# Kernel optimization log

Measured on AMD Instinct MI355X. Metric: run time of the kernel, lower is better.

The kernel has to match this reference:

```python
import jax, jax.numpy as jnp
import numpy as np
from jax import lax

EPS = 1e-6  # LayerNorm2d eps


def _ln2d(x, w, b):
    # channel-wise LayerNorm over dim 1 of [B,C,H,W]
    mu = jnp.mean(x, axis=1, keepdims=True)
    var = jnp.mean((x - mu) ** 2, axis=1, keepdims=True)
    return (x - mu) / jnp.sqrt(var + EPS) * w[None, :, None, None] + b[None, :, None, None]


def _conv1x1(x, w, b):
    # w: [O, C]
    return jnp.einsum('bchw,oc->bohw', x, w) + b[None, :, None, None]


def _dconv(x, w, b):
    # 3x3 conv, dilation 4, padding 4 -> same H,W. w: [O, C, 3, 3]
    y = lax.conv_general_dilated(x, w, window_strides=(1, 1),
                                 padding=((4, 4), (4, 4)), rhs_dilation=(4, 4),
                                 dimension_numbers=('NCHW', 'OIHW', 'NCHW'))
    return y + b[None, :, None, None]


def _forward(x_l, x_r, nl_w, nl_b, nr_w, nr_b, lp1_w, lp1_b, rp1_w, rp1_b,
             dl_w, dl_b, dr_w, dr_b, lp2_w, lp2_b, rp2_w, rp2_b, beta, gamma):
    c = x_l.shape[1]
    scale = c ** (-0.5)
    N_l = _ln2d(x_l, nl_w, nl_b)
    N_r = _ln2d(x_r, nr_w, nr_b)
    V_l = jnp.transpose(_conv1x1(x_l, lp2_w, lp2_b), (0, 2, 3, 1))   # [B,H,W,C]
    V_r = jnp.transpose(_conv1x1(x_r, rp2_w, rp2_b), (0, 2, 3, 1))
    Q_l = jnp.transpose(_conv1x1(N_l, lp1_w, lp1_b), (0, 2, 3, 1))   # [B,H,W,C]
    Q_r = jnp.transpose(_conv1x1(N_r, rp1_w, rp1_b), (0, 2, 3, 1))
    K_l_T = jnp.transpose(_dconv(N_l, dl_w, dl_b), (0, 2, 1, 3))     # [B,H,C,W]
    K_r_T = jnp.transpose(_dconv(N_r, dr_w, dr_b), (0, 2, 1, 3))
    # per-row cross attention: [B,H,W,W]
    attn_r2l = jnp.einsum('bhwc,bhcv->bhwv', Q_l, K_r_T) * scale
    attn_l2r = jnp.einsum('bhwc,bhcv->bhwv', Q_r, K_l_T) * scale
    F_r2l = jnp.einsum('bhwv,bhvc->bhwc', jax.nn.softmax(attn_r2l, axis=-1), V_r)
    F_l2r = jnp.einsum('bhwv,bhvc->bhwc', jax.nn.softmax(attn_l2r, axis=-1), V_l)
    F_r2l = jnp.transpose(F_r2l, (0, 3, 1, 2)) * beta   # [B,C,H,W]
    F_l2r = jnp.transpose(F_l2r, (0, 3, 1, 2)) * gamma
    return x_l + F_r2l, x_r + F_l2r


def setup_inputs() -> dict:
    key = jax.random.key(0)
    ks = jax.random.split(key, 12)
    B, C, H, W = 2, 128, 192, 512
    s = 0.02
    rn = lambda k, shp: s * jax.random.normal(k, shp, jnp.float32)
    return {
        'x_l': jax.random.normal(ks[0], (B, C, H, W), jnp.float32),
        'x_r': jax.random.normal(ks[1], (B, C, H, W), jnp.float32),
        'nl_w': jnp.ones((C,), jnp.float32), 'nl_b': jnp.zeros((C,), jnp.float32),
        'nr_w': jnp.ones((C,), jnp.float32), 'nr_b': jnp.zeros((C,), jnp.float32),
        'lp1_w': rn(ks[2], (C, C)), 'lp1_b': jnp.zeros((C,), jnp.float32),
        'rp1_w': rn(ks[3], (C, C)), 'rp1_b': jnp.zeros((C,), jnp.float32),
        'dl_w': rn(ks[4], (C, C, 3, 3)), 'dl_b': jnp.zeros((C,), jnp.float32),
        'dr_w': rn(ks[5], (C, C, 3, 3)), 'dr_b': jnp.zeros((C,), jnp.float32),
        'lp2_w': rn(ks[6], (C, C)), 'lp2_b': jnp.zeros((C,), jnp.float32),
        'rp2_w': rn(ks[7], (C, C)), 'rp2_b': jnp.zeros((C,), jnp.float32),
        'beta': 0.1 * jax.random.normal(ks[8], (1, C, 1, 1), jnp.float32),
        'gamma': 0.1 * jax.random.normal(ks[9], (1, C, 1, 1), jnp.float32),
    }


def reference(x_l, x_r, nl_w, nl_b, nr_w, nr_b, lp1_w, lp1_b, rp1_w, rp1_b,
              dl_w, dl_b, dr_w, dr_b, lp2_w, lp2_b, rp2_w, rp2_b, beta, gamma):
    return _forward(x_l, x_r, nl_w, nl_b, nr_w, nr_b, lp1_w, lp1_b, rp1_w, rp1_b,
                    dl_w, dl_b, dr_w, dr_b, lp2_w, lp2_b, rp2_w, rp2_b, beta, gamma)
```

## Files before the change

### kernel.cpp

```cpp
#include <hip/hip_runtime.h>
#include <stdint.h>

#define CC 128
#define HH 192
#define WW 512
#define BB 2
#define HW (HH*WW)
#define CHW (CC*HW)
#define TENS (BB*CHW)

typedef __attribute__((ext_vector_type(8))) short bf16x8;
typedef __attribute__((ext_vector_type(4))) float f32x4;
typedef __attribute__((ext_vector_type(4))) unsigned short u16x4;

__device__ __forceinline__ unsigned short f2bf(float f) {
    union { float f; unsigned u; } v; v.f = f;
    return (unsigned short)((v.u + 0x7FFFu + ((v.u >> 16) & 1u)) >> 16);
}
__device__ __forceinline__ float bf2f(unsigned short u) {
    union { unsigned u; float f; } v; v.u = ((unsigned)u) << 16;
    return v.f;
}
__device__ __forceinline__ uint32_t cvtpk(float lo, float hi) {
    uint32_t r;
    asm("v_cvt_pk_bf16_f32 %0, %1, %2" : "=v"(r) : "v"(lo), "v"(hi));
    return r;
}
__device__ __forceinline__ f32x4 MFMA(bf16x8 a, bf16x8 b, f32x4 c) {
    return __builtin_amdgcn_mfma_f32_16x16x32_bf16(a, b, c, 0, 0, 0);
}

__global__ __launch_bounds__(256) void wcast_k(
    const float* __restrict__ dlw, const float* __restrict__ drw,
    unsigned short* __restrict__ wd)
{
    int i = blockIdx.x * 256 + threadIdx.x;
    if (i >= 2 * 9 * CC * CC) return;
    int side = i / (9 * CC * CC);
    int r = i % (9 * CC * CC);
    int tap = r / (CC * CC);
    int r2 = r % (CC * CC);
    int o = r2 >> 7, c = r2 & 127;
    const float* src = side ? drw : dlw;
    wd[i] = f2bf(src[((size_t)o * CC + c) * 9 + tap]);
}

__global__ __launch_bounds__(256) void lnv_k(
    const float* __restrict__ xl, const float* __restrict__ xr,
    const float* __restrict__ nlw, const float* __restrict__ nlb,
    const float* __restrict__ nrw, const float* __restrict__ nrb,
    const float* __restrict__ wlp, const float* __restrict__ blp,
    const float* __restrict__ wrp, const float* __restrict__ brp,
    unsigned short* __restrict__ ntl, unsigned short* __restrict__ ntr,
    unsigned short* __restrict__ vlo, unsigned short* __restrict__ vro)
{
    const int side = blockIdx.y;
    const float* x  = side ? xr : xl;
    const float* nw = side ? nrw : nlw;
    const float* nb = side ? nrb : nlb;
    const float* wv = side ? wrp : wlp;
    const float* bv = side ? brp : blp;
    unsigned short* nt = side ? ntr : ntl;
    unsigned short* vo = side ? vro : vlo;
    const int bid = blockIdx.x;
    const int wt = bid & 7, h = (bid >> 3) % HH, b = bid / (8 * HH);
    const int w0 = wt * 64;
    const int t = threadIdx.x;

    __shared__ unsigned short sA[64][136];
    __shared__ unsigned short sB[128][136];
    __shared__ float red[8][64];
    __shared__ float smu[64], srs[64];

    {
        const int w = t & 63, cg = t >> 6;
        const float* xp = x + (size_t)b * CHW + (size_t)h * WW + w0 + w;
        float s = 0.f, q = 0.f;
        for (int i = 0; i < 16; i++) {
            int c = cg * 32 + i * 2;
            float v0 = xp[(size_t)c * HW];
            float v1 = xp[(size_t)(c + 1) * HW];
            ushort2 u; u.x = f2bf(v0); u.y = f2bf(v1);
            *(ushort2*)&sA[w][c] = u;
            s += v0 + v1; q += v0 * v0 + v1 * v1;
        }
        red[cg][w] = s; red[4 + cg][w] = q;
    }
    for (int it = 0; it < 16; it++) {
        int f = it * 1024 + t * 4;
        int o = f >> 7, c = f & 127;
        float4 v = *(const float4*)(wv + o * CC + c);
        sB[o][c] = f2bf(v.x); sB[o][c + 1] = f2bf(v.y);
        sB[o][c + 2] = f2bf(v.z); sB[o][c + 3] = f2bf(v.w);
    }
    __syncthreads();
    if (t < 64) {
        float S = red[0][t] + red[1][t] + red[2][t] + red[3][t];
        float Q = red[4][t] + red[5][t] + red[6][t] + red[7][t];
        float mu = S * (1.f / CC);
        float var = fmaxf(Q * (1.f / CC) - mu * mu, 0.f);
        smu[t] = mu; srs[t] = rsqrtf(var + 1e-6f);
    }
    __syncthreads();
    {
        const int w = t >> 2, c0 = (t & 3) * 32;
        const float mu = smu[w], rs = srs[w];
        unsigned short* np = nt + ((size_t)(b * HH + h) * WW + w0 + w) * CC;
        for (int i = 0; i < 32; i += 2) {
            int c = c0 + i;
            float v0 = (bf2f(sA[w][c]) - mu) * rs * nw[c] + nb[c];
            float v1 = (bf2f(sA[w][c + 1]) - mu) * rs * nw[c + 1] + nb[c + 1];
            ushort2 u; u.x = f2bf(v0); u.y = f2bf(v1);
            *(ushort2*)&np[c] = u;
        }
    }
    const int wid = t >> 6, l = t & 63, lr = l & 15, lg = l >> 4;
    f32x4 acc[8] = {};
    for (int kk = 0; kk < 4; kk++) {
        bf16x8 a = *(const bf16x8*)&sA[wid * 16 + lr][kk * 32 + lg * 8];
#pragma unroll
        for (int n_ = 0; n_ < 8; n_++) {
            bf16x8 bb = *(const bf16x8*)&sB[n_ * 16 + lr][kk * 32 + lg * 8];
            acc[n_] = MFMA(a, bb, acc[n_]);
        }
    }
    unsigned short* vp = vo + ((size_t)(b * HH + h) * CC) * WW + w0;
    for (int n_ = 0; n_ < 8; n_++) {
        int o = n_ * 16 + lr;
        float bias = bv[o];
        u16x4 u;
        u[0] = f2bf(acc[n_][0] + bias);
        u[1] = f2bf(acc[n_][1] + bias);
        u[2] = f2bf(acc[n_][2] + bias);
        u[3] = f2bf(acc[n_][3] + bias);
        *(u16x4*)&vp[(size_t)o * WW + wid * 16 + lg * 4] = u;
    }
}

__global__ __launch_bounds__(256) void dconv_k(
    const unsigned short* __restrict__ ntl, const unsigned short* __restrict__ ntr,
    const unsigned short* __restrict__ wd,
    const float* __restrict__ dlb, const float* __restrict__ drb,
    unsigned short* __restrict__ klo, unsigned short* __restrict__ kro)
{
    const int side = blockIdx.y;
    const unsigned short* nt = side ? ntr : ntl;
    const unsigned short* wdp = wd + (size_t)side * 9 * CC * CC;
    const float* bd = side ? drb : dlb;
    unsigned short* ko = side ? kro : klo;
    const int bid0 = blockIdx.x;
    const int lgc = (bid0 & 7) * 192 + (bid0 >> 3);
    const int wt = lgc & 3;
    const int hb = lgc >> 2;
    const int h = hb % HH, b = hb / HH;
    const int w0 = wt * 128;
    const int t = threadIdx.x;
    const int wid = t >> 6, l = t & 63, lr = l & 15, lg = l >> 4;

    __shared__ unsigned short sA[136][136];
    __shared__ unsigned short sB[128][136];

    f32x4 acc[2][8] = {};
    for (int dy = 0; dy < 3; dy++) {
        const int hh = h + 4 * (dy - 1);
        const bool hok = (hh >= 0 && hh < HH);
        __syncthreads();
        for (int f = t * 8; f < 136 * 128; f += 2048) {
            int wloc = f >> 7, c = f & 127;
            int w = w0 - 4 + wloc;
            bf16x8 v = {0, 0, 0, 0, 0, 0, 0, 0};
            if (hok && w >= 0 && w < WW)
                v = *(const bf16x8*)(nt + ((size_t)(b * HH + hh) * WW + w) * CC + c);
            *(bf16x8*)&sA[wloc][c] = v;
        }
        for (int dx = 0; dx < 3; dx++) {
            __syncthreads();
            const int tap = dy * 3 + dx;
            for (int it = 0; it < 8; it++) {
                int f = it * 2048 + t * 8;
                *(bf16x8*)&sB[f >> 7][f & 127] =
                    *(const bf16x8*)(wdp + (size_t)tap * CC * CC + f);
            }
            __syncthreads();
            const int ar = wid * 16 + lr + 4 * dx;
            for (int kk = 0; kk < 4; kk++) {
                bf16x8 a0 = *(const bf16x8*)&sA[ar][kk * 32 + lg * 8];
                bf16x8 a1 = *(const bf16x8*)&sA[64 + ar][kk * 32 + lg * 8];
#pragma unroll
                for (int n_ = 0; n_ < 8; n_++) {
                    bf16x8 bb = *(const bf16x8*)&sB[n_ * 16 + lr][kk * 32 + lg * 8];
                    acc[0][n_] = MFMA(a0, bb, acc[0][n_]);
                    acc[1][n_] = MFMA(a1, bb, acc[1][n_]);
                }
            }
        }
    }
    unsigned short* kp = ko + ((size_t)(b * HH + h) * WW + w0) * CC;
    for (int mi = 0; mi < 2; mi++)
        for (int n_ = 0; n_ < 8; n_++) {
            int o = n_ * 16 + lr;
            float bias = bd[o];
            for (int j = 0; j < 4; j++) {
                int w = mi * 64 + wid * 16 + lg * 4 + j;
                kp[(size_t)w * CC + o] = f2bf(acc[mi][n_][j] + bias);
            }
        }
}

__global__ __launch_bounds__(256, 3) void attn_k(
    const unsigned short* __restrict__ ntl, const unsigned short* __restrict__ ntr,
    const unsigned short* __restrict__ kl,  const unsigned short* __restrict__ kr,
    const unsigned short* __restrict__ vtl, const unsigned short* __restrict__ vtr,
    const float* __restrict__ lp1w, const float* __restrict__ lp1b,
    const float* __restrict__ rp1w, const float* __restrict__ rp1b,
    const float* __restrict__ xl, const float* __restrict__ xr,
    const float* __restrict__ beta, const float* __restrict__ gamma,
    float* __restrict__ out)
{
    __shared__ __align__(16) char smem[53248];
    unsigned short* sQ  = (unsigned short*)smem;
    unsigned short* sW  = (unsigned short*)(smem + 17408);
    unsigned short* sKt = (unsigned short*)(smem + 17408);
    unsigned short* sVt = (unsigned short*)(smem + 34816);

    const int dir = blockIdx.z;
    const unsigned short* nq  = dir ? ntr : ntl;
    const unsigned short* kws = dir ? kl : kr;
    const unsigned short* vws = dir ? vtl : vtr;
    const float* wq   = dir ? rp1w : lp1w;
    const float* bq   = dir ? rp1b : lp1b;
    const float* xres = dir ? xr : xl;
    const float* mult = dir ? gamma : beta;
    float* op = out + (size_t)dir * TENS;

    const int bid = blockIdx.x;
    const int xcd = bid & 7;
    const int s   = bid >> 3;
    const int qb  = s & 7;
    const int bh  = xcd + 8 * (s >> 3);
    const int q0  = qb * 64;
    const int t = threadIdx.x;
    const int wid = t >> 6, l = t & 63, lr = l & 15, lg = l >> 4;

    const unsigned short* ksrc = kws + (size_t)bh * WW * CC;
    const unsigned short* vsrc = vws + (size_t)bh * CC * WW;

    bf16x8 kreg[4], vreg[4];
#pragma unroll
    for (int it = 0; it < 4; it++) {
        int f = it * 2048 + t * 8;
        kreg[it] = *(const bf16x8*)(ksrc + f);
    }
#pragma unroll
    for (int it = 0; it < 4; it++) {
        int f = it * 2048 + t * 8;
        int c = f >> 6, k = f & 63;
        vreg[it] = *(const bf16x8*)(vsrc + (size_t)c * WW + k);
    }

    {
        const unsigned short* nsrc = nq + ((size_t)bh * WW + q0) * CC;
        for (int it = 0; it < 4; it++) {
            int f = it * 2048 + t * 8;
            *(bf16x8*)&sQ[(f >> 7) * 136 + (f & 127)] = *(const bf16x8*)(nsrc + f);
        }
        for (int it = 0; it < 16; it++) {
            int f = it * 1024 + t * 4;
            int o = f >> 7, c = f & 127;
            float4 v = *(const float4*)(wq + o * CC + c);
            unsigned short* p = &sW[o * 136 + c];
            p[0] = f2bf(v.x); p[1] = f2bf(v.y); p[2] = f2bf(v.z); p[3] = f2bf(v.w);
        }
    }
    __syncthreads();
    f32x4 qacc[8] = {};
    for (int kk = 0; kk < 4; kk++) {
        bf16x8 a = *(const bf16x8*)&sQ[(wid * 16 + lr) * 136 + kk * 32 + lg * 8];
#pragma unroll
        for (int n_ = 0; n_ < 8; n_++) {
            bf16x8 b = *(const bf16x8*)&sW[(n_ * 16 + lr) * 136 + kk * 32 + lg * 8];
            qacc[n_] = MFMA(a, b, qacc[n_]);
        }
    }
    const float SCL = 0.08838834764831845f * 1.4426950408889634f;
    for (int n_ = 0; n_ < 8; n_++) {
        float bias = bq[n_ * 16 + lr];
        for (int j = 0; j < 4; j++)
            sQ[(wid * 16 + lg * 4 + j) * 136 + n_ * 16 + lr] =
                f2bf((qacc[n_][j] + bias) * SCL);
    }
    __syncthreads();
    bf16x8 qf[4];
#pragma unroll
    for (int kk = 0; kk < 4; kk++)
        qf[kk] = *(const bf16x8*)&sQ[(wid * 16 + lr) * 136 + kk * 32 + lg * 8];

    f32x4 oacc[8] = {};
    float mrow = -1e30f, lrow = 0.f;
    const int src0 = lr + ((l & 16) << 1);
    const int src1 = src0 + 16;
    const int hi = lg >> 1;

    for (int kb = 0; kb < 8; kb++) {
        __syncthreads();
#pragma unroll
        for (int it = 0; it < 4; it++) {
            int f = it * 2048 + t * 8;
            *(bf16x8*)&sKt[(f >> 7) * 136 + (f & 127)] = kreg[it];
        }
#pragma unroll
        for (int it = 0; it < 4; it++) {
            int f = it * 2048 + t * 8;
            int c = f >> 6, k = f & 63;
            *(bf16x8*)&sVt[c * 72 + k] = vreg[it];
        }
        if (kb < 7) {
#pragma unroll
            for (int it = 0; it < 4; it++) {
                int f = it * 2048 + t * 8;
                kreg[it] = *(const bf16x8*)(ksrc + (kb + 1) * 64 * CC + f);
            }
#pragma unroll
            for (int it = 0; it < 4; it++) {
                int f = it * 2048 + t * 8;
                int c = f >> 6, k = f & 63;
                vreg[it] = *(const bf16x8*)(vsrc + (size_t)c * WW + (kb + 1) * 64 + k);
            }
        }
        __syncthreads();
        f32x4 sacc[4] = {};
        __builtin_amdgcn_s_setprio(1);
        for (int kk = 0; kk < 4; kk++)
#pragma unroll
            for (int n_ = 0; n_ < 4; n_++) {
                bf16x8 kf = *(const bf16x8*)&sKt[(n_ * 16 + lr) * 136 + kk * 32 + lg * 8];
                sacc[n_] = MFMA(kf, qf[kk], sacc[n_]);
            }
        __builtin_amdgcn_s_setprio(0);
        float pm = sacc[0][0];
#pragma unroll
        for (int n_ = 0; n_ < 4; n_++)
#pragma unroll
            for (int j = 0; j < 4; j++) pm = fmaxf(pm, sacc[n_][j]);
        pm = fmaxf(pm, __shfl_xor(pm, 16, 64));
        pm = fmaxf(pm, __shfl_xor(pm, 32, 64));
        float mn = fmaxf(mrow, pm);
        float al = exp2f(mrow - mn);
        mrow = mn;
        float p[4][4];
        float rs = 0.f;
#pragma unroll
        for (int n_ = 0; n_ < 4; n_++)
#pragma unroll
            for (int j = 0; j < 4; j++) {
                p[n_][j] = exp2f(sacc[n_][j] - mn);
                rs += p[n_][j];
            }
        rs += __shfl_xor(rs, 16, 64);
        rs += __shfl_xor(rs, 32, 64);
        lrow = lrow * al + rs;
#pragma unroll
        for (int n_ = 0; n_ < 8; n_++) {
            f32x4 o = oacc[n_];
            o[0] *= al; o[1] *= al; o[2] *= al; o[3] *= al;
            oacc[n_] = o;
        }
        uint32_t pa0 = cvtpk(p[0][0], p[0][1]), pa1 = cvtpk(p[0][2], p[0][3]);
        uint32_t pb0 = cvtpk(p[1][0], p[1][1]), pb1 = cvtpk(p[1][2], p[1][3]);
        uint32_t pc0 = cvtpk(p[2][0], p[2][1]), pc1 = cvtpk(p[2][2], p[2][3]);
        uint32_t pd0 = cvtpk(p[3][0], p[3][1]), pd1 = cvtpk(p[3][2], p[3][3]);
        {
            uint32_t q00 = __shfl(pa0, src0, 64);
            uint32_t q01 = __shfl(pa1, src0, 64);
            uint32_t q02 = __shfl(pa0, src1, 64);
            uint32_t q03 = __shfl(pa1, src1, 64);
            uint32_t q10 = __shfl(pb0, src0, 64);
            uint32_t q11 = __shfl(pb1, src0, 64);
            uint32_t q12 = __shfl(pb0, src1, 64);
            uint32_t q13 = __shfl(pb1, src1, 64);
            union { uint32_t u[4]; bf16x8 v; } pf;
            pf.u[0] = hi ? q10 : q00;
            pf.u[1] = hi ? q11 : q01;
            pf.u[2] = hi ? q12 : q02;
            pf.u[3] = hi ? q13 : q03;
            __builtin_amdgcn_s_setprio(1);
#pragma unroll
            for (int n_ = 0; n_ < 8; n_++) {
                bf16x8 va = *(const bf16x8*)&sVt[(n_ * 16 + lr) * 72 + lg * 8];
                oacc[n_] = MFMA(va, pf.v, oacc[n_]);
            }
            __builtin_amdgcn_s_setprio(0);
        }
        {
            uint32_t q00 = __shfl(pc0, src0, 64);
            uint32_t q01 = __shfl(pc1, src0, 64);
            uint32_t q02 = __shfl(pc0, src1, 64);
            uint32_t q03 = __shfl(pc1, src1, 64);
            uint32_t q10 = __shfl(pd0, src0, 64);
            uint32_t q11 = __shfl(pd1, src0, 64);
            uint32_t q12 = __shfl(pd0, src1, 64);
            uint32_t q13 = __shfl(pd1, src1, 64);
            union { uint32_t u[4]; bf16x8 v; } pf;
            pf.u[0] = hi ? q10 : q00;
            pf.u[1] = hi ? q11 : q01;
            pf.u[2] = hi ? q12 : q02;
            pf.u[3] = hi ? q13 : q03;
            __builtin_amdgcn_s_setprio(1);
#pragma unroll
            for (int n_ = 0; n_ < 8; n_++) {
                bf16x8 va = *(const bf16x8*)&sVt[(n_ * 16 + lr) * 72 + 32 + lg * 8];
                oacc[n_] = MFMA(va, pf.v, oacc[n_]);
            }
            __builtin_amdgcn_s_setprio(0);
        }
    }

    const float inv = 1.f / lrow;
    const int b = bh / HH, h = bh % HH;
    const int w = q0 + wid * 16 + lr;
    const float* xp = xres + (size_t)b * CHW + (size_t)h * WW + w;
    float* outp = op + (size_t)b * CHW + (size_t)h * WW + w;
#pragma unroll
    for (int n_ = 0; n_ < 8; n_++)
#pragma unroll
        for (int j = 0; j < 4; j++) {
            int c = n_ * 16 + lg * 4 + j;
            outp[(size_t)c * HW] = xp[(size_t)c * HW] + oacc[n_][j] * inv * mult[c];
        }
}

extern "C" void kernel_launch(void* const* d_in, const int* in_sizes, int n_in,
                              void* d_out, int out_size, void* d_ws, size_t ws_size,
                              hipStream_t stream)
{
    const float* xl   = (const float*)d_in[0];
    const float* xr   = (const float*)d_in[1];
    const float* nlw  = (const float*)d_in[2];
    const float* nlb  = (const float*)d_in[3];
    const float* nrw  = (const float*)d_in[4];
    const float* nrb  = (const float*)d_in[5];
    const float* lp1w = (const float*)d_in[6];
    const float* lp1b = (const float*)d_in[7];
    const float* rp1w = (const float*)d_in[8];
    const float* rp1b = (const float*)d_in[9];
    const float* dlw  = (const float*)d_in[10];
    const float* dlb  = (const float*)d_in[11];
    const float* drw  = (const float*)d_in[12];
    const float* drb  = (const float*)d_in[13];
    const float* lp2w = (const float*)d_in[14];
    const float* lp2b = (const float*)d_in[15];
    const float* rp2w = (const float*)d_in[16];
    const float* rp2b = (const float*)d_in[17];
    const float* beta = (const float*)d_in[18];
    const float* gamma= (const float*)d_in[19];
    float* out = (float*)d_out;

    unsigned short* ws = (unsigned short*)d_ws;
    const size_t A = (size_t)TENS;
    unsigned short* Ntl = ws;
    unsigned short* Ntr = ws + A;
    unsigned short* Kl  = ws + 2 * A;
    unsigned short* Kr  = ws + 3 * A;
    unsigned short* Vtl = ws + 4 * A;
    unsigned short* Vtr = ws + 5 * A;
    unsigned short* Wd  = ws + 6 * A;

    wcast_k<<<dim3(1152), 256, 0, stream>>>(dlw, drw, Wd);
    lnv_k<<<dim3(3072, 2), 256, 0, stream>>>(xl, xr, nlw, nlb, nrw, nrb,
        lp2w, lp2b, rp2w, rp2b, Ntl, Ntr, Vtl, Vtr);
    dconv_k<<<dim3(1536, 2), 256, 0, stream>>>(Ntl, Ntr, Wd, dlb, drb, Kl, Kr);
    attn_k<<<dim3(3072, 1, 2), 256, 0, stream>>>(Ntl, Ntr, Kl, Kr, Vtl, Vtr,
        lp1w, lp1b, rp1w, rp1b, xl, xr, beta, gamma, out);
}
```

Before: 578.5 us.

## Double attention query tile per block and retile dconv warps as 2x2 output grid

The attention kernel now handles 128 queries per block (32 per warp, two MFMA query groups), so each staged K/V tile is reused across twice as many queries and the grid is halved. Shared memory grows and launch bounds drop to 2 blocks per CU. The dconv kernel splits warps into a 2x2 grid over width and output channels, loading 4 A and 4 B fragments for 16 MFMAs instead of 2 A and 8 B. Scalar bf16 conversions are replaced with packed cvtpk stores in several places.

```diff
diff --git a/kernel.cpp b/kernel.cpp
--- a/kernel.cpp
+++ b/kernel.cpp
@@ -80,8 +80,7 @@
             int c = cg * 32 + i * 2;
             float v0 = xp[(size_t)c * HW];
             float v1 = xp[(size_t)(c + 1) * HW];
-            ushort2 u; u.x = f2bf(v0); u.y = f2bf(v1);
-            *(ushort2*)&sA[w][c] = u;
+            *(uint32_t*)&sA[w][c] = cvtpk(v0, v1);
             s += v0 + v1; q += v0 * v0 + v1 * v1;
         }
         red[cg][w] = s; red[4 + cg][w] = q;
@@ -90,8 +89,8 @@
         int f = it * 1024 + t * 4;
         int o = f >> 7, c = f & 127;
         float4 v = *(const float4*)(wv + o * CC + c);
-        sB[o][c] = f2bf(v.x); sB[o][c + 1] = f2bf(v.y);
-        sB[o][c + 2] = f2bf(v.z); sB[o][c + 3] = f2bf(v.w);
+        *(uint32_t*)&sB[o][c]     = cvtpk(v.x, v.y);
+        *(uint32_t*)&sB[o][c + 2] = cvtpk(v.z, v.w);
     }
     __syncthreads();
     if (t < 64) {
@@ -110,8 +109,7 @@
             int c = c0 + i;
             float v0 = (bf2f(sA[w][c]) - mu) * rs * nw[c] + nb[c];
             float v1 = (bf2f(sA[w][c + 1]) - mu) * rs * nw[c + 1] + nb[c + 1];
-            ushort2 u; u.x = f2bf(v0); u.y = f2bf(v1);
-            *(ushort2*)&np[c] = u;
+            *(uint32_t*)&np[c] = cvtpk(v0, v1);
         }
     }
     const int wid = t >> 6, l = t & 63, lr = l & 15, lg = l >> 4;
@@ -128,12 +126,10 @@
     for (int n_ = 0; n_ < 8; n_++) {
         int o = n_ * 16 + lr;
         float bias = bv[o];
-        u16x4 u;
-        u[0] = f2bf(acc[n_][0] + bias);
-        u[1] = f2bf(acc[n_][1] + bias);
-        u[2] = f2bf(acc[n_][2] + bias);
-        u[3] = f2bf(acc[n_][3] + bias);
-        *(u16x4*)&vp[(size_t)o * WW + wid * 16 + lg * 4] = u;
+        uint2 uu;
+        uu.x = cvtpk(acc[n_][0] + bias, acc[n_][1] + bias);
+        uu.y = cvtpk(acc[n_][2] + bias, acc[n_][3] + bias);
+        *(uint2*)&vp[(size_t)o * WW + wid * 16 + lg * 4] = uu;
     }
 }
 
@@ -156,11 +152,12 @@
     const int w0 = wt * 128;
     const int t = threadIdx.x;
     const int wid = t >> 6, l = t & 63, lr = l & 15, lg = l >> 4;
+    const int whalf = wid & 1, ohalf = wid >> 1;
 
     __shared__ unsigned short sA[136][136];
     __shared__ unsigned short sB[128][136];
 
-    f32x4 acc[2][8] = {};
+    f32x4 acc[4][4] = {};
     for (int dy = 0; dy < 3; dy++) {
         const int hh = h + 4 * (dy - 1);
         const bool hok = (hh >= 0 && hh < HH);
@@ -182,32 +179,35 @@
                     *(const bf16x8*)(wdp + (size_t)tap * CC * CC + f);
             }
             __syncthreads();
-            const int ar = wid * 16 + lr + 4 * dx;
             for (int kk = 0; kk < 4; kk++) {
-                bf16x8 a0 = *(const bf16x8*)&sA[ar][kk * 32 + lg * 8];
-                bf16x8 a1 = *(const bf16x8*)&sA[64 + ar][kk * 32 + lg * 8];
-#pragma unroll
-                for (int n_ = 0; n_ < 8; n_++) {
-                    bf16x8 bb = *(const bf16x8*)&sB[n_ * 16 + lr][kk * 32 + lg * 8];
-                    acc[0][n_] = MFMA(a0, bb, acc[0][n_]);
-                    acc[1][n_] = MFMA(a1, bb, acc[1][n_]);
-                }
+                bf16x8 af[4], bf_[4];
+#pragma unroll
+                for (int g = 0; g < 4; g++)
+                    af[g] = *(const bf16x8*)&sA[whalf * 64 + g * 16 + lr + 4 * dx][kk * 32 + lg * 8];
+#pragma unroll
+                for (int n_ = 0; n_ < 4; n_++)
+                    bf_[n_] = *(const bf16x8*)&sB[ohalf * 64 + n_ * 16 + lr][kk * 32 + lg * 8];
+#pragma unroll
+                for (int g = 0; g < 4; g++)
+#pragma unroll
+                    for (int n_ = 0; n_ < 4; n_++)
+                        acc[g][n_] = MFMA(af[g], bf_[n_], acc[g][n_]);
             }
         }
     }
     unsigned short* kp = ko + ((size_t)(b * HH + h) * WW + w0) * CC;
-    for (int mi = 0; mi < 2; mi++)
-        for (int n_ = 0; n_ < 8; n_++) {
-            int o = n_ * 16 + lr;
+    for (int g = 0; g < 4; g++)
+        for (int n_ = 0; n_ < 4; n_++) {
+            int o = ohalf * 64 + n_ * 16 + lr;
             float bias = bd[o];
             for (int j = 0; j < 4; j++) {
-                int w = mi * 64 + wid * 16 + lg * 4 + j;
-                kp[(size_t)w * CC + o] = f2bf(acc[mi][n_][j] + bias);
-            }
-        }
-}
-
-__global__ __launch_bounds__(256, 3) void attn_k(
+                int w = whalf * 64 + g * 16 + lg * 4 + j;
+                kp[(size_t)w * CC + o] = f2bf(acc[g][n_][j] + bias);
+            }
+        }
+}
+
+__global__ __launch_bounds__(256, 2) void attn_k(
     const unsigned short* __restrict__ ntl, const unsigned short* __restrict__ ntr,
     const unsigned short* __restrict__ kl,  const unsigned short* __restrict__ kr,
     const unsigned short* __restrict__ vtl, const unsigned short* __restrict__ vtr,
@@ -217,11 +217,11 @@
     const float* __restrict__ beta, const float* __restrict__ gamma,
     float* __restrict__ out)
 {
-    __shared__ __align__(16) char smem[53248];
+    __shared__ __align__(16) char smem[70656];
     unsigned short* sQ  = (unsigned short*)smem;
-    unsigned short* sW  = (unsigned short*)(smem + 17408);
-    unsigned short* sKt = (unsigned short*)(smem + 17408);
-    unsigned short* sVt = (unsigned short*)(smem + 34816);
+    unsigned short* sW  = (unsigned short*)(smem + 34816);
+    unsigned short* sKt = (unsigned short*)(smem + 34816);
+    unsigned short* sVt = (unsigned short*)(smem + 52224);
 
     const int dir = blockIdx.z;
     const unsigned short* nq  = dir ? ntr : ntl;
@@ -236,9 +236,9 @@
     const int bid = blockIdx.x;
     const int xcd = bid & 7;
     const int s   = bid >> 3;
-    const int qb  = s & 7;
-    const int bh  = xcd + 8 * (s >> 3);
-    const int q0  = qb * 64;
+    const int qb  = s & 3;
+    const int bh  = xcd + 8 * (s >> 2);
+    const int q0  = qb * 128;
     const int t = threadIdx.x;
     const int wid = t >> 6, l = t & 63, lr = l & 15, lg = l >> 4;
 
@@ -260,7 +260,7 @@
 
     {
         const unsigned short* nsrc = nq + ((size_t)bh * WW + q0) * CC;
-        for (int it = 0; it < 4; it++) {
+        for (int it = 0; it < 8; it++) {
             int f = it * 2048 + t * 8;
             *(bf16x8*)&sQ[(f >> 7) * 136 + (f & 127)] = *(const bf16x8*)(nsrc + f);
         }
@@ -268,35 +268,47 @@
             int f = it * 1024 + t * 4;
             int o = f >> 7, c = f & 127;
             float4 v = *(const float4*)(wq + o * CC + c);
-            unsigned short* p = &sW[o * 136 + c];
-            p[0] = f2bf(v.x); p[1] = f2bf(v.y); p[2] = f2bf(v.z); p[3] = f2bf(v.w);
+            *(uint32_t*)&sW[o * 136 + c]     = cvtpk(v.x, v.y);
+            *(uint32_t*)&sW[o * 136 + c + 2] = cvtpk(v.z, v.w);
         }
     }
     __syncthreads();
-    f32x4 qacc[8] = {};
-    for (int kk = 0; kk < 4; kk++) {
-        bf16x8 a = *(const bf16x8*)&sQ[(wid * 16 + lr) * 136 + kk * 32 + lg * 8];
-#pragma unroll
-        for (int n_ = 0; n_ < 8; n_++) {
-            bf16x8 b = *(const bf16x8*)&sW[(n_ * 16 + lr) * 136 + kk * 32 + lg * 8];
-            qacc[n_] = MFMA(a, b, qacc[n_]);
-        }
-    }
-    const float SCL = 0.08838834764831845f * 1.4426950408889634f;
-    for (int n_ = 0; n_ < 8; n_++) {
-        float bias = bq[n_ * 16 + lr];
-        for (int j = 0; j < 4; j++)
-            sQ[(wid * 16 + lg * 4 + j) * 136 + n_ * 16 + lr] =
-                f2bf((qacc[n_][j] + bias) * SCL);
+    {
+        f32x4 qacc[2][8] = {};
+        for (int kk = 0; kk < 4; kk++) {
+            bf16x8 a0 = *(const bf16x8*)&sQ[(wid * 32 + lr) * 136 + kk * 32 + lg * 8];
+            bf16x8 a1 = *(const bf16x8*)&sQ[(wid * 32 + 16 + lr) * 136 + kk * 32 + lg * 8];
+#pragma unroll
+            for (int n_ = 0; n_ < 8; n_++) {
+                bf16x8 b = *(const bf16x8*)&sW[(n_ * 16 + lr) * 136 + kk * 32 + lg * 8];
+                qacc[0][n_] = MFMA(a0, b, qacc[0][n_]);
+                qacc[1][n_] = MFMA(a1, b, qacc[1][n_]);
+            }
+        }
+        const float SCL = 0.08838834764831845f * 1.4426950408889634f;
+        __syncthreads();
+#pragma unroll
+        for (int mg = 0; mg < 2; mg++)
+#pragma unroll
+            for (int n_ = 0; n_ < 8; n_++) {
+                float bias = bq[n_ * 16 + lr];
+#pragma unroll
+                for (int j = 0; j < 4; j++)
+                    sQ[(wid * 32 + mg * 16 + lg * 4 + j) * 136 + n_ * 16 + lr] =
+                        f2bf((qacc[mg][n_][j] + bias) * SCL);
+            }
     }
     __syncthreads();
-    bf16x8 qf[4];
-#pragma unroll
-    for (int kk = 0; kk < 4; kk++)
-        qf[kk] = *(const bf16x8*)&sQ[(wid * 16 + lr) * 136 + kk * 32 + lg * 8];
-
-    f32x4 oacc[8] = {};
-    float mrow = -1e30f, lrow = 0.f;
+    bf16x8 qf[2][4];
+#pragma unroll
+    for (int qg = 0; qg < 2; qg++)
+#pragma unroll
+        for (int kk = 0; kk < 4; kk++)
+            qf[qg][kk] = *(const bf16x8*)&sQ[(wid * 32 + qg * 16 + lr) * 136 + kk * 32 + lg * 8];
+
+    f32x4 oacc[8][2] = {};
+    float mrow[2] = {-1e30f, -1e30f};
+    float lrow[2] = {0.f, 0.f};
     const int src0 = lr + ((l & 16) << 1);
     const int src1 = src0 + 16;
     const int hi = lg >> 1;
@@ -328,105 +340,103 @@
             }
         }
         __syncthreads();
-        f32x4 sacc[4] = {};
+        f32x4 sacc[2][4] = {};
         __builtin_amdgcn_s_setprio(1);
         for (int kk = 0; kk < 4; kk++)
 #pragma unroll
             for (int n_ = 0; n_ < 4; n_++) {
                 bf16x8 kf = *(const bf16x8*)&sKt[(n_ * 16 + lr) * 136 + kk * 32 + lg * 8];
-                sacc[n_] = MFMA(kf, qf[kk], sacc[n_]);
+                sacc[0][n_] = MFMA(kf, qf[0][kk], sacc[0][n_]);
+                sacc[1][n_] = MFMA(kf, qf[1][kk], sacc[1][n_]);
             }
         __builtin_amdgcn_s_setprio(0);
-        float pm = sacc[0][0];
-#pragma unroll
-        for (int n_ = 0; n_ < 4; n_++)
-#pragma unroll
-            for (int j = 0; j < 4; j++) pm = fmaxf(pm, sacc[n_][j]);
-        pm = fmaxf(pm, __shfl_xor(pm, 16, 64));
-        pm = fmaxf(pm, __shfl_xor(pm, 32, 64));
-        float mn = fmaxf(mrow, pm);
-        float al = exp2f(mrow - mn);
-        mrow = mn;
-        float p[4][4];
-        float rs = 0.f;
-#pragma unroll
-        for (int n_ = 0; n_ < 4; n_++)
-#pragma unroll
-            for (int j = 0; j < 4; j++) {
-                p[n_][j] = exp2f(sacc[n_][j] - mn);
-                rs += p[n_][j];
-            }
-        rs += __shfl_xor(rs, 16, 64);
-        rs += __shfl_xor(rs, 32, 64);
-        lrow = lrow * al + rs;
-#pragma unroll
-        for (int n_ = 0; n_ < 8; n_++) {
-            f32x4 o = oacc[n_];
-            o[0] *= al; o[1] *= al; o[2] *= al; o[3] *= al;
-            oacc[n_] = o;
-        }
-        uint32_t pa0 = cvtpk(p[0][0], p[0][1]), pa1 = cvtpk(p[0][2], p[0][3]);
-        uint32_t pb0 = cvtpk(p[1][0], p[1][1]), pb1 = cvtpk(p[1][2], p[1][3]);
-        uint32_t pc0 = cvtpk(p[2][0], p[2][1]), pc1 = cvtpk(p[2][2], p[2][3]);
-        uint32_t pd0 = cvtpk(p[3][0], p[3][1]), pd1 = cvtpk(p[3][2], p[3][3]);
-        {
-            uint32_t q00 = __shfl(pa0, src0, 64);
-            uint32_t q01 = __shfl(pa1, src0, 64);
-            uint32_t q02 = __shfl(pa0, src1, 64);
-            uint32_t q03 = __shfl(pa1, src1, 64);
-            uint32_t q10 = __shfl(pb0, src0, 64);
-            uint32_t q11 = __shfl(pb1, src0, 64);
-            uint32_t q12 = __shfl(pb0, src1, 64);
-            uint32_t q13 = __shfl(pb1, src1, 64);
-            union { uint32_t u[4]; bf16x8 v; } pf;
-            pf.u[0] = hi ? q10 : q00;
-            pf.u[1] = hi ? q11 : q01;
-            pf.u[2] = hi ? q12 : q02;
-            pf.u[3] = hi ? q13 : q03;
+        float al[2];
+#pragma unroll
+        for (int qg = 0; qg < 2; qg++) {
+            float pm = sacc[qg][0][0];
+#pragma unroll
+            for (int n_ = 0; n_ < 4; n_++)
+#pragma unroll
+                for (int j = 0; j < 4; j++) pm = fmaxf(pm, sacc[qg][n_][j]);
+            pm = fmaxf(pm, __shfl_xor(pm, 16, 64));
+            pm = fmaxf(pm, __shfl_xor(pm, 32, 64));
+            float mn = fmaxf(mrow[qg], pm);
+            al[qg] = exp2f(mrow[qg] - mn);
+            mrow[qg] = mn;
+            float rs = 0.f;
+#pragma unroll
+            for (int n_ = 0; n_ < 4; n_++)
+#pragma unroll
+                for (int j = 0; j < 4; j++) {
+                    float e = exp2f(sacc[qg][n_][j] - mn);
+                    sacc[qg][n_][j] = e;
+                    rs += e;
+                }
+            rs += __shfl_xor(rs, 16, 64);
+            rs += __shfl_xor(rs, 32, 64);
+            lrow[qg] = lrow[qg] * al[qg] + rs;
+        }
+#pragma unroll
+        for (int n_ = 0; n_ < 8; n_++)
+#pragma unroll
+            for (int qg = 0; qg < 2; qg++) {
+                f32x4 o = oacc[n_][qg];
+                o[0] *= al[qg]; o[1] *= al[qg]; o[2] *= al[qg]; o[3] *= al[qg];
+                oacc[n_][qg] = o;
+            }
+        uint32_t pk[2][4][2];
+#pragma unroll
+        for (int qg = 0; qg < 2; qg++)
+#pragma unroll
+            for (int n_ = 0; n_ < 4; n_++) {
+                pk[qg][n_][0] = cvtpk(sacc[qg][n_][0], sacc[qg][n_][1]);
+                pk[qg][n_][1] = cvtpk(sacc[qg][n_][2], sacc[qg][n_][3]);
+            }
+#pragma unroll
+        for (int kk = 0; kk < 2; kk++) {
+            union { uint32_t u[4]; bf16x8 v; } pf[2];
+#pragma unroll
+            for (int qg = 0; qg < 2; qg++) {
+                uint32_t q00 = __shfl(pk[qg][kk * 2][0],     src0, 64);
+                uint32_t q01 = __shfl(pk[qg][kk * 2][1],     src0, 64);
+                uint32_t q02 = __shfl(pk[qg][kk * 2][0],     src1, 64);
+                uint32_t q03 = __shfl(pk[qg][kk * 2][1],     src1, 64);
+                uint32_t q10 = __shfl(pk[qg][kk * 2 + 1][0], src0, 64);
+                uint32_t q11 = __shfl(pk[qg][kk * 2 + 1][1], src0, 64);
+                uint32_t q12 = __shfl(pk[qg][kk * 2 + 1][0], src1, 64);
+                uint32_t q13 = __shfl(pk[qg][kk * 2 + 1][1], src1, 64);
+                pf[qg].u[0] = hi ? q10 : q00;
+                pf[qg].u[1] = hi ? q11 : q01;
+                pf[qg].u[2] = hi ? q12 : q02;
+                pf[qg].u[3] = hi ? q13 : q03;
+            }
             __builtin_amdgcn_s_setprio(1);
 #pragma unroll
             for (int n_ = 0; n_ < 8; n_++) {
-                bf16x8 va = *(const bf16x8*)&sVt[(n_ * 16 + lr) * 72 + lg * 8];
-                oacc[n_] = MFMA(va, pf.v, oacc[n_]);
+                bf16x8 va = *(const bf16x8*)&sVt[(n_ * 16 + lr) * 72 + kk * 32 + lg * 8];
+                oacc[n_][0] = MFMA(va, pf[0].v, oacc[n_][0]);
+                oacc[n_][1] = MFMA(va, pf[1].v, oacc[n_][1]);
             }
             __builtin_amdgcn_s_setprio(0);
         }
-        {
-            uint32_t q00 = __shfl(pc0, src0, 64);
-            uint32_t q01 = __shfl(pc1, src0, 64);
-            uint32_t q02 = __shfl(pc0, src1, 64);
-            uint32_t q03 = __shfl(pc1, src1, 64);
-            uint32_t q10 = __shfl(pd0, src0, 64);
-            uint32_t q11 = __shfl(pd1, src0, 64);
-            uint32_t q12 = __shfl(pd0, src1, 64);
-            uint32_t q13 = __shfl(pd1, src1, 64);
-            union { uint32_t u[4]; bf16x8 v; } pf;
-            pf.u[0] = hi ? q10 : q00;
-            pf.u[1] = hi ? q11 : q01;
-            pf.u[2] = hi ? q12 : q02;
-            pf.u[3] = hi ? q13 : q03;
-            __builtin_amdgcn_s_setprio(1);
-#pragma unroll
-            for (int n_ = 0; n_ < 8; n_++) {
-                bf16x8 va = *(const bf16x8*)&sVt[(n_ * 16 + lr) * 72 + 32 + lg * 8];
-                oacc[n_] = MFMA(va, pf.v, oacc[n_]);
-            }
-            __builtin_amdgcn_s_setprio(0);
-        }
-    }
-
-    const float inv = 1.f / lrow;
+    }
+
+    const float inv0 = 1.f / lrow[0], inv1 = 1.f / lrow[1];
     const int b = bh / HH, h = bh % HH;
-    const int w = q0 + wid * 16 + lr;
-    const float* xp = xres + (size_t)b * CHW + (size_t)h * WW + w;
-    float* outp = op + (size_t)b * CHW + (size_t)h * WW + w;
-#pragma unroll
-    for (int n_ = 0; n_ < 8; n_++)
+    const int w_0 = q0 + wid * 32 + lr;
+    const float* xp0 = xres + (size_t)b * CHW + (size_t)h * WW + w_0;
+    float* outp0 = op + (size_t)b * CHW + (size_t)h * WW + w_0;
+#pragma unroll
+    for (int n_ = 0; n_ < 8; n_++) {
+        float4 m4 = *(const float4*)&mult[n_ * 16 + lg * 4];
 #pragma unroll
         for (int j = 0; j < 4; j++) {
             int c = n_ * 16 + lg * 4 + j;
-            outp[(size_t)c * HW] = xp[(size_t)c * HW] + oacc[n_][j] * inv * mult[c];
-        }
+            float mj = (&m4.x)[j];
+            outp0[(size_t)c * HW]      = xp0[(size_t)c * HW]      + oacc[n_][0][j] * inv0 * mj;
+            outp0[(size_t)c * HW + 16] = xp0[(size_t)c * HW + 16] + oacc[n_][1][j] * inv1 * mj;
+        }
+    }
 }
 
 extern "C" void kernel_launch(void* const* d_in, const int* in_sizes, int n_in,
@@ -469,6 +479,6 @@
     lnv_k<<<dim3(3072, 2), 256, 0, stream>>>(xl, xr, nlw, nlb, nrw, nrb,
         lp2w, lp2b, rp2w, rp2b, Ntl, Ntr, Vtl, Vtr);
     dconv_k<<<dim3(1536, 2), 256, 0, stream>>>(Ntl, Ntr, Wd, dlb, drb, Kl, Kr);
-    attn_k<<<dim3(3072, 1, 2), 256, 0, stream>>>(Ntl, Ntr, Kl, Kr, Vtl, Vtr,
+    attn_k<<<dim3(1536, 1, 2), 256, 0, stream>>>(Ntl, Ntr, Kl, Kr, Vtl, Vtr,
         lp1w, lp1b, rp1w, rp1b, xl, xr, beta, gamma, out);
 }
```

Measured after the change: 547.6 us. 1.06x faster.
